# Optimization experiments

Hardware: AMD Instinct MI355X
Metric: run time of the kernel (lower is better)

The kernel has to match this reference:

```python
import jax, jax.numpy as jnp
import numpy as np

D_MODEL = 1024
D_STATE = 16
D_CONV = 4
EXPAND = 2
D_INNER = EXPAND * D_MODEL
BATCH = 2
SEQ = 4096


def setup_inputs() -> dict:
    key = jax.random.key(0)
    ks = jax.random.split(key, 8)
    def w(k, shape, fan_in):
        return jax.random.normal(k, shape, jnp.float32) * (fan_in ** -0.5)
    x = jax.random.normal(ks[0], (BATCH, SEQ, D_MODEL), jnp.float32)
    in_proj_w = w(ks[1], (2 * D_INNER, D_MODEL), D_MODEL)
    conv_w = w(ks[2], (D_INNER, 1, D_CONV), D_CONV)          # depthwise conv kernel (OIH, groups=D_INNER)
    conv_b = jnp.zeros((D_INNER,), jnp.float32)
    x_proj_w = w(ks[3], (1 + 2 * D_STATE, D_INNER), D_INNER)
    dt_proj_w = w(ks[4], (D_INNER, 1), D_STATE)               # Linear(1 -> d_inner), see notes
    dt_proj_b = jnp.zeros((D_INNER,), jnp.float32)
    A_log = jnp.log(jnp.tile(jnp.arange(1, D_STATE + 1, dtype=jnp.float32)[None, :], (D_INNER, 1)))
    D = jnp.ones((D_INNER,), jnp.float32)
    out_proj_w = w(ks[5], (D_MODEL, D_INNER), D_INNER)
    return dict(x=x, in_proj_w=in_proj_w, conv_w=conv_w, conv_b=conv_b,
                x_proj_w=x_proj_w, dt_proj_w=dt_proj_w, dt_proj_b=dt_proj_b,
                A_log=A_log, D=D, out_proj_w=out_proj_w)


def _selective_scan(xs, delta, Bm, Cm, A, D):
    # xs, delta: [B, L, d_inner]; Bm, Cm: [B, L, d_state]; A: [d_inner, d_state]
    def step(h, inp):
        x_t, d_t, b_t, c_t = inp                      # [B,di],[B,di],[B,n],[B,n]
        dA = jnp.exp(d_t[..., None] * A)              # [B, di, n]
        h = dA * h + (d_t * x_t)[..., None] * b_t[:, None, :]
        y = jnp.einsum('bdn,bn->bd', h, c_t) + D * x_t
        return h, y
    h0 = jnp.zeros((xs.shape[0], xs.shape[2], A.shape[1]), xs.dtype)
    seq = (jnp.swapaxes(xs, 0, 1), jnp.swapaxes(delta, 0, 1),
           jnp.swapaxes(Bm, 0, 1), jnp.swapaxes(Cm, 0, 1))
    _, ys = jax.lax.scan(step, h0, seq)               # ys: [L, B, di]
    return jnp.swapaxes(ys, 0, 1)


def _mamba(x, in_proj_w, conv_w, conv_b, x_proj_w, dt_proj_w, dt_proj_b, A_log, D, out_proj_w):
    xz = x @ in_proj_w.T                               # [B, L, 2*di]
    xc, z = jnp.split(xz, 2, axis=-1)
    # causal depthwise conv (pad left d_conv-1, truncate to seq_len)
    u = jnp.swapaxes(xc, 1, 2)                         # [B, di, L]
    u = jax.lax.conv_general_dilated(
        u, conv_w, window_strides=(1,), padding=[(D_CONV - 1, 0)],
        feature_group_count=D_INNER, dimension_numbers=('NCH', 'OIH', 'NCH'))
    u = u + conv_b[None, :, None]
    xs = jax.nn.silu(jnp.swapaxes(u, 1, 2))            # [B, L, di]
    dbc = xs @ x_proj_w.T                              # [B, L, 1+2n]
    delta_raw = dbc[..., :1]
    Bm = dbc[..., 1:1 + D_STATE]
    Cm = dbc[..., 1 + D_STATE:]
    delta = jax.nn.softplus(delta_raw @ dt_proj_w.T + dt_proj_b)   # [B, L, di]
    A = -jnp.exp(A_log)
    y = _selective_scan(xs, delta, Bm, Cm, A, D)
    return (y * jax.nn.silu(z)) @ out_proj_w.T


def reference(x, in_proj_w, conv_w, conv_b, x_proj_w, dt_proj_w, dt_proj_b, A_log, D, out_proj_w):
    return _mamba(x, in_proj_w, conv_w, conv_b, x_proj_w, dt_proj_w, dt_proj_b, A_log, D, out_proj_w)
```

## Files before the change

### kernel.cpp

```cpp
#include <hip/hip_runtime.h>
#include <hip/hip_bf16.h>
#include <stdint.h>

typedef __bf16 bf16x8 __attribute__((ext_vector_type(8)));
typedef float  f32x4  __attribute__((ext_vector_type(4)));
typedef unsigned short u16x8 __attribute__((ext_vector_type(8)));

#define TC 64
#define NC 64
#define TH 32

__device__ __forceinline__ unsigned short f2bf(float f) {
  unsigned u = __builtin_bit_cast(unsigned, f);
  unsigned r = (u + 0x7fffu + ((u >> 16) & 1u)) >> 16;
  return (unsigned short)r;
}
__device__ __forceinline__ float bf2f(unsigned short s) {
  unsigned u = ((unsigned)s) << 16;
  return __builtin_bit_cast(float, u);
}

__device__ __forceinline__ void gload_lds16(const void* g, void* l) {
  __builtin_amdgcn_global_load_lds(
      (const __attribute__((address_space(1))) unsigned int*)(g),
      (__attribute__((address_space(3))) unsigned int*)(l),
      16, 0, 0);
}

__device__ __forceinline__ void rpowers(float r, float* rp) {
  float r2 = r * r, r4 = r2 * r2, r8 = r4 * r4;
  rp[0] = r;        rp[1] = r2;       rp[2] = r2 * r;   rp[3] = r4;
  rp[4] = r4 * r;   rp[5] = r4 * r2;  rp[6] = rp[5] * r; rp[7] = r8;
  rp[8] = r8 * r;   rp[9] = r8 * r2;  rp[10] = rp[9] * r; rp[11] = r8 * r4;
  rp[12] = rp[11] * r; rp[13] = rp[11] * r2; rp[14] = rp[13] * r; rp[15] = r8 * r8;
}

__global__ __launch_bounds__(256) void cast_bf16_k(const float4* __restrict__ in,
                                                   ushort4* __restrict__ out, int n4) {
  int i = blockIdx.x * 256 + threadIdx.x;
  int stride = gridDim.x * 256;
  for (; i < n4; i += stride) {
    float4 v = in[i];
    ushort4 o;
    o.x = f2bf(v.x); o.y = f2bf(v.y); o.z = f2bf(v.z); o.w = f2bf(v.w);
    out[i] = o;
  }
}

__global__ __launch_bounds__(256) void pad_xw_k(const float* __restrict__ xw,
                                                unsigned short* __restrict__ xwp) {
  int i = blockIdx.x * 256 + threadIdx.x;
  if (i >= 128 * 2048) return;
  int row = i >> 11, col = i & 2047;
  xwp[i] = (row < 33) ? f2bf(xw[row * 2048 + col]) : (unsigned short)0;
}

template <bool BF16OUT>
__global__ __launch_bounds__(256) void gemm_bf16_nt(
    const unsigned short* __restrict__ A, const unsigned short* __restrict__ B,
    void* __restrict__ Cv, int M, int N, int K)
{
  __shared__ __align__(16) unsigned short As[128 * 32];
  __shared__ __align__(16) unsigned short Bs[128 * 32];
  const int tid = threadIdx.x;
  const int m0 = blockIdx.x * 128;
  const int n0 = blockIdx.y * 128;
  const int w = tid >> 6, l = tid & 63;
  const int wr = w >> 1, wc = w & 1;
  const int lr = l & 15, kk = (l >> 4) * 8;

  f32x4 acc[4][4];
#pragma unroll
  for (int mi = 0; mi < 4; ++mi)
#pragma unroll
    for (int ni = 0; ni < 4; ++ni)
      acc[mi][ni] = (f32x4){0.f, 0.f, 0.f, 0.f};

  for (int k0 = 0; k0 < K; k0 += 32) {
#pragma unroll
    for (int i = 0; i < 2; ++i) {
      int q = tid + 256 * i;
      int row = q >> 2, sub = q & 3;
      gload_lds16(A + (size_t)(m0 + row) * K + k0 + sub * 8, &As[q * 8]);
      gload_lds16(B + (size_t)(n0 + row) * K + k0 + sub * 8, &Bs[q * 8]);
    }
    __syncthreads();
    bf16x8 af[4], bfr[4];
#pragma unroll
    for (int mi = 0; mi < 4; ++mi)
      af[mi] = *(const bf16x8*)&As[(wr * 64 + mi * 16 + lr) * 32 + kk];
#pragma unroll
    for (int ni = 0; ni < 4; ++ni)
      bfr[ni] = *(const bf16x8*)&Bs[(wc * 64 + ni * 16 + lr) * 32 + kk];
#pragma unroll
    for (int mi = 0; mi < 4; ++mi)
#pragma unroll
      for (int ni = 0; ni < 4; ++ni)
        acc[mi][ni] = __builtin_amdgcn_mfma_f32_16x16x32_bf16(af[mi], bfr[ni], acc[mi][ni], 0, 0, 0);
    __syncthreads();
  }

#pragma unroll
  for (int mi = 0; mi < 4; ++mi)
#pragma unroll
    for (int ni = 0; ni < 4; ++ni) {
      int gr = m0 + wr * 64 + mi * 16 + (l >> 4) * 4;
      int gc = n0 + wc * 64 + ni * 16 + (l & 15);
#pragma unroll
      for (int j = 0; j < 4; ++j) {
        if (BF16OUT)
          ((unsigned short*)Cv)[(size_t)(gr + j) * N + gc] = f2bf(acc[mi][ni][j]);
        else
          ((float*)Cv)[(size_t)(gr + j) * N + gc] = acc[mi][ni][j];
      }
    }
}

#define KSPLIT 4
__global__ __launch_bounds__(256) void gemm_bf16_splitk(
    const unsigned short* __restrict__ A, const unsigned short* __restrict__ B,
    float* __restrict__ Cpart, int M, int N, int K)
{
  __shared__ __align__(16) unsigned short As[128 * 32];
  __shared__ __align__(16) unsigned short Bs[128 * 32];
  const int tid = threadIdx.x;
  const int m0 = blockIdx.x * 128;
  const int n0 = 0;
  const int z = blockIdx.z;
  const int kseg = K / KSPLIT;
  const int kbeg = z * kseg;
  const int w = tid >> 6, l = tid & 63;
  const int wr = w >> 1, wc = w & 1;
  const int lr = l & 15, kk = (l >> 4) * 8;
  float* C = Cpart + (size_t)z * M * N;

  f32x4 acc[4][4];
#pragma unroll
  for (int mi = 0; mi < 4; ++mi)
#pragma unroll
    for (int ni = 0; ni < 4; ++ni)
      acc[mi][ni] = (f32x4){0.f, 0.f, 0.f, 0.f};

  for (int k0 = kbeg; k0 < kbeg + kseg; k0 += 32) {
#pragma unroll
    for (int i = 0; i < 2; ++i) {
      int q = tid + 256 * i;
      int row = q >> 2, sub = q & 3;
      gload_lds16(A + (size_t)(m0 + row) * K + k0 + sub * 8, &As[q * 8]);
      gload_lds16(B + (size_t)(n0 + row) * K + k0 + sub * 8, &Bs[q * 8]);
    }
    __syncthreads();
    bf16x8 af[4], bfr[4];
#pragma unroll
    for (int mi = 0; mi < 4; ++mi)
      af[mi] = *(const bf16x8*)&As[(wr * 64 + mi * 16 + lr) * 32 + kk];
#pragma unroll
    for (int ni = 0; ni < 4; ++ni)
      bfr[ni] = *(const bf16x8*)&Bs[(wc * 64 + ni * 16 + lr) * 32 + kk];
#pragma unroll
    for (int mi = 0; mi < 4; ++mi)
#pragma unroll
      for (int ni = 0; ni < 4; ++ni)
        acc[mi][ni] = __builtin_amdgcn_mfma_f32_16x16x32_bf16(af[mi], bfr[ni], acc[mi][ni], 0, 0, 0);
    __syncthreads();
  }

#pragma unroll
  for (int mi = 0; mi < 4; ++mi)
#pragma unroll
    for (int ni = 0; ni < 4; ++ni) {
      int gr = m0 + wr * 64 + mi * 16 + (l >> 4) * 4;
      int gc = n0 + wc * 64 + ni * 16 + (l & 15);
#pragma unroll
      for (int j = 0; j < 4; ++j)
        C[(size_t)(gr + j) * N + gc] = acc[mi][ni][j];
    }
}

__global__ __launch_bounds__(256) void redux4_k(const float4* __restrict__ part,
                                                float4* __restrict__ out) {
  int i = blockIdx.x * 256 + threadIdx.x;
  const int STR = 262144;
  float4 a = part[i], b = part[i + STR], c = part[i + 2 * STR], d = part[i + 3 * STR];
  out[i] = make_float4(a.x + b.x + c.x + d.x, a.y + b.y + c.y + d.y,
                       a.z + b.z + c.z + d.z, a.w + b.w + c.w + d.w);
}

#define CONV_L 16
__global__ __launch_bounds__(256) void conv_silu_k(
    const unsigned short* __restrict__ xzb, const float* __restrict__ cw,
    const float* __restrict__ cb, unsigned short* __restrict__ xsb)
{
  const int b = blockIdx.y;
  const int l0 = blockIdx.x * CONV_L;
  const int d = threadIdx.x * 8;
  float w[4][8], bias[8];
#pragma unroll
  for (int i = 0; i < 8; ++i) {
    bias[i] = cb[d + i];
#pragma unroll
    for (int j = 0; j < 4; ++j) w[j][i] = cw[(d + i) * 4 + j];
  }
  const size_t rb = (size_t)b * 4096;
  float win[3][8];
#pragma unroll
  for (int j = 0; j < 3; ++j) {
    int l = l0 - 3 + j;
    if (l >= 0) {
      u16x8 v = *(const u16x8*)(xzb + (rb + l) * 4096 + d);
#pragma unroll
      for (int i = 0; i < 8; ++i) win[j][i] = bf2f(v[i]);
    } else {
#pragma unroll
      for (int i = 0; i < 8; ++i) win[j][i] = 0.f;
    }
  }
  for (int l = l0; l < l0 + CONV_L; ++l) {
    u16x8 v = *(const u16x8*)(xzb + (rb + l) * 4096 + d);
    float cur[8]; u16x8 ob;
#pragma unroll
    for (int i = 0; i < 8; ++i) {
      cur[i] = bf2f(v[i]);
      float u = bias[i] + w[0][i] * win[0][i] + w[1][i] * win[1][i]
                        + w[2][i] * win[2][i] + w[3][i] * cur[i];
      float s = u / (1.f + __expf(-u));
      ob[i] = f2bf(s);
    }
    *(u16x8*)(xsb + (rb + l) * 2048 + d) = ob;
#pragma unroll
    for (int i = 0; i < 8; ++i) { win[0][i] = win[1][i]; win[1][i] = win[2][i]; win[2][i] = cur[i]; }
  }
}

__global__ __launch_bounds__(256) void scan_p1(
    const unsigned short* __restrict__ xsb16, const float* __restrict__ dbc,
    const float* __restrict__ dtw, const float* __restrict__ dtb,
    const float* __restrict__ alog,
    float* __restrict__ Sg, float* __restrict__ cdg)
{
  const int chunk = blockIdx.x;
  const int d0 = blockIdx.y * 256;
  const int b = blockIdx.z;
  const int tid = threadIdx.x;
  const size_t rowbase = (size_t)b * 4096 + chunk * TC;

  __shared__ __align__(16) unsigned short xsS[TH][256];
  __shared__ __align__(16) float bS[TC][16];
  __shared__ float drS[TC];

  if (tid < TC) drS[tid] = dbc[(rowbase + tid) * 128];
  for (int i = tid; i < TC * 16; i += 256) {
    int t = i >> 4, q = i & 15;
    bS[t][q] = dbc[(rowbase + t) * 128 + 1 + q];
  }

  const int d = d0 + tid;
  const float wdt = dtw[d], bdt = dtb[d];
  float adn[16];
  bool ok = true;
#pragma unroll
  for (int k = 0; k < 4; ++k) {
    float4 a4 = *(const float4*)(alog + (size_t)d * 16 + k * 4);
    adn[4 * k + 0] = -__expf(a4.x); adn[4 * k + 1] = -__expf(a4.y);
    adn[4 * k + 2] = -__expf(a4.z); adn[4 * k + 3] = -__expf(a4.w);
  }
#pragma unroll
  for (int n = 0; n < 16; ++n)
    ok = ok && (fabsf(adn[n] + (float)(n + 1)) <= 1e-3f * (float)(n + 1));

  float h[16];
#pragma unroll
  for (int n = 0; n < 16; ++n) h[n] = 0.f;
  float cd = 0.f;

  for (int half = 0; half < 2; ++half) {
    if (half) __syncthreads();
    for (int i = tid; i < TH * 32; i += 256) {
      int tt = i >> 5, q = i & 31;
      *(u16x8*)&xsS[tt][q * 8] =
          *(const u16x8*)(xsb16 + (rowbase + half * TH + tt) * 2048 + d0 + q * 8);
    }
    __syncthreads();

    if (ok) {
      for (int tt = 0; tt < TH; ++tt) {
        int t = half * TH + tt;
        float pre = fmaf(drS[t], wdt, bdt);
        float e = __expf(pre);
        float dlt = (pre > 20.f) ? pre : __logf(1.f + e);
        float xv = bf2f(xsS[tt][tid]);
        float dx = dlt * xv;
        cd += dlt;
        float r = __expf(-dlt);
        float rp[16];
        rpowers(r, rp);
        f32x4 Bv[4];
#pragma unroll
        for (int k = 0; k < 4; ++k) Bv[k] = ((const f32x4*)&bS[t][0])[k];
#pragma unroll
        for (int n = 0; n < 16; ++n)
          h[n] = fmaf(rp[n], h[n], dx * Bv[n >> 2][n & 3]);
      }
    } else {
      for (int tt = 0; tt < TH; ++tt) {
        int t = half * TH + tt;
        float pre = fmaf(drS[t], wdt, bdt);
        float e = __expf(pre);
        float dlt = (pre > 20.f) ? pre : __logf(1.f + e);
        float xv = bf2f(xsS[tt][tid]);
        float dx = dlt * xv;
        cd += dlt;
        f32x4 Bv[4];
#pragma unroll
        for (int k = 0; k < 4; ++k) Bv[k] = ((const f32x4*)&bS[t][0])[k];
#pragma unroll
        for (int n = 0; n < 16; ++n) {
          float dA = __expf(adn[n] * dlt);
          h[n] = fmaf(dA, h[n], dx * Bv[n >> 2][n & 3]);
        }
      }
    }
  }
  cdg[(size_t)(b * NC + chunk) * 2048 + d] = cd;
  float* Sp = Sg + ((size_t)(b * NC + chunk) * 32768 + (size_t)d * 16);
#pragma unroll
  for (int k = 0; k < 4; ++k)
    ((float4*)Sp)[k] = make_float4(h[4 * k], h[4 * k + 1], h[4 * k + 2], h[4 * k + 3]);
}

__global__ __launch_bounds__(256) void scan_p2(
    const float* __restrict__ Sg, const float* __restrict__ cdg,
    const float* __restrict__ alog, float* __restrict__ Hg)
{
  int g = blockIdx.x * 256 + threadIdx.x;
  int b = g >> 15, dn = g & 32767;
  int d = dn >> 4;
  float adn = -__expf(alog[dn]);
  float h = 0.f;
  for (int c = 0; c < NC; ++c) {
    size_t o = (size_t)(b * NC + c) * 32768 + dn;
    float P = __expf(adn * cdg[(size_t)(b * NC + c) * 2048 + d]);
    Hg[o] = h;
    h = fmaf(P, h, Sg[o]);
  }
}

__global__ __launch_bounds__(256) void scan_p3(
    const unsigned short* __restrict__ xsb16, const float* __restrict__ dbc,
    const float* __restrict__ dtw, const float* __restrict__ dtb,
    const float* __restrict__ alog, const float* __restrict__ Dp,
    const unsigned short* __restrict__ xzb, const float* __restrict__ Hg,
    unsigned short* __restrict__ gb)
{
  const int chunk = blockIdx.x;
  const int d0 = blockIdx.y * 256;
  const int b = blockIdx.z;
  const int tid = threadIdx.x;
  const size_t rowbase = (size_t)b * 4096 + chunk * TC;

  __shared__ __align__(16) unsigned short xsS[TH][256];
  __shared__ __align__(16) float bcS[TC][32];

  for (int i = tid; i < TC * 32; i += 256) {
    int t = i >> 5, q = i & 31;
    bcS[t][q] = dbc[(rowbase + t) * 128 + 1 + q];
  }

  const int d = d0 + tid;
  const float wdt = dtw[d], bdt = dtb[d], Dd = Dp[d];
  const float* __restrict__ drp = dbc + rowbase * 128;
  float adn[16];
  bool ok = true;
#pragma unroll
  for (int k = 0; k < 4; ++k) {
    float4 a4 = *(const float4*)(alog + (size_t)d * 16 + k * 4);
    adn[4 * k + 0] = -__expf(a4.x); adn[4 * k + 1] = -__expf(a4.y);
    adn[4 * k + 2] = -__expf(a4.z); adn[4 * k + 3] = -__expf(a4.w);
  }
#pragma unroll
  for (int n = 0; n < 16; ++n)
    ok = ok && (fabsf(adn[n] + (float)(n + 1)) <= 1e-3f * (float)(n + 1));

  float h[16];
  {
    const float* Hp = Hg + ((size_t)(b * NC + chunk) * 32768 + (size_t)d * 16);
#pragma unroll
    for (int k = 0; k < 4; ++k) {
      float4 h4 = ((const float4*)Hp)[k];
      h[4 * k + 0] = h4.x; h[4 * k + 1] = h4.y; h[4 * k + 2] = h4.z; h[4 * k + 3] = h4.w;
    }
  }

  for (int half = 0; half < 2; ++half) {
    if (half) __syncthreads();
    for (int i = tid; i < TH * 32; i += 256) {
      int tt = i >> 5, q = i & 31;
      *(u16x8*)&xsS[tt][q * 8] =
          *(const u16x8*)(xsb16 + (rowbase + half * TH + tt) * 2048 + d0 + q * 8);
    }
    __syncthreads();

    if (ok) {
      for (int tt = 0; tt < TH; ++tt) {
        int t = half * TH + tt;
        float pre = fmaf(drp[(size_t)t * 128], wdt, bdt);
        float e = __expf(pre);
        float dlt = (pre > 20.f) ? pre : __logf(1.f + e);
        float xv = bf2f(xsS[tt][tid]);
        float dx = dlt * xv;
        float r = __expf(-dlt);
        float rp[16];
        rpowers(r, rp);
        f32x4 Bv[4], Cv[4];
#pragma unroll
        for (int k = 0; k < 4; ++k) {
          Bv[k] = ((const f32x4*)&bcS[t][0])[k];
          Cv[k] = ((const f32x4*)&bcS[t][16])[k];
        }
        float yp[4];
        yp[0] = Dd * xv; yp[1] = 0.f; yp[2] = 0.f; yp[3] = 0.f;
#pragma unroll
        for (int n = 0; n < 16; ++n) {
          h[n] = fmaf(rp[n], h[n], dx * Bv[n >> 2][n & 3]);
          yp[n & 3] = fmaf(h[n], Cv[n >> 2][n & 3], yp[n & 3]);
        }
        float y = (yp[0] + yp[1]) + (yp[2] + yp[3]);
        xsS[tt][tid] = f2bf(y);
      }
    } else {
      for (int tt = 0; tt < TH; ++tt) {
        int t = half * TH + tt;
        float pre = fmaf(drp[(size_t)t * 128], wdt, bdt);
        float e = __expf(pre);
        float dlt = (pre > 20.f) ? pre : __logf(1.f + e);
        float xv = bf2f(xsS[tt][tid]);
        float dx = dlt * xv;
        f32x4 Bv[4], Cv[4];
#pragma unroll
        for (int k = 0; k < 4; ++k) {
          Bv[k] = ((const f32x4*)&bcS[t][0])[k];
          Cv[k] = ((const f32x4*)&bcS[t][16])[k];
        }
        float yp[4];
        yp[0] = Dd * xv; yp[1] = 0.f; yp[2] = 0.f; yp[3] = 0.f;
#pragma unroll
        for (int n = 0; n < 16; ++n) {
          float dA = __expf(adn[n] * dlt);
          h[n] = fmaf(dA, h[n], dx * Bv[n >> 2][n & 3]);
          yp[n & 3] = fmaf(h[n], Cv[n >> 2][n & 3], yp[n & 3]);
        }
        float y = (yp[0] + yp[1]) + (yp[2] + yp[3]);
        xsS[tt][tid] = f2bf(y);
      }
    }
    __syncthreads();

    for (int i = tid; i < TH * 32; i += 256) {
      int tt = i >> 5, q = i & 31;
      size_t row = rowbase + half * TH + tt;
      u16x8 yv = *(const u16x8*)&xsS[tt][q * 8];
      u16x8 zv = *(const u16x8*)(xzb + row * 4096 + 2048 + d0 + q * 8);
      u16x8 ov;
#pragma unroll
      for (int j = 0; j < 8; ++j) {
        float z = bf2f(zv[j]);
        float s = z / (1.f + __expf(-z));
        ov[j] = f2bf(bf2f(yv[j]) * s);
      }
      *(u16x8*)(gb + row * 2048 + d0 + q * 8) = ov;
    }
  }
}

extern "C" void kernel_launch(void* const* d_in, const int* in_sizes, int n_in,
                              void* d_out, int out_size, void* d_ws, size_t ws_size,
                              hipStream_t stream) {
  const float* x    = (const float*)d_in[0];
  const float* ipw  = (const float*)d_in[1];
  const float* cw   = (const float*)d_in[2];
  const float* cb   = (const float*)d_in[3];
  const float* xpw  = (const float*)d_in[4];
  const float* dtw  = (const float*)d_in[5];
  const float* dtb  = (const float*)d_in[6];
  const float* alog = (const float*)d_in[7];
  const float* Dp   = (const float*)d_in[8];
  const float* opw  = (const float*)d_in[9];
  float* out = (float*)d_out;

  char* p = (char*)d_ws;
  unsigned short* xb   = (unsigned short*)p; p += (size_t)8388608 * 2;
  unsigned short* wb1  = (unsigned short*)p; p += (size_t)4194304 * 2;
  unsigned short* wb2  = (unsigned short*)p; p += (size_t)2097152 * 2;
  unsigned short* xwp  = (unsigned short*)p; p += (size_t)262144 * 2;
  unsigned short* xzb  = (unsigned short*)p; p += (size_t)33554432 * 2;
  unsigned short* xsb16= (unsigned short*)p; p += (size_t)16777216 * 2;
  float*          dbc  = (float*)p;          p += (size_t)1048576 * 4;
  unsigned short* gb   = (unsigned short*)p; p += (size_t)16777216 * 2;
  float*          Sg   = (float*)p;          p += (size_t)4194304 * 4;
  float*          cdg  = (float*)p;          p += (size_t)262144 * 4;
  float*          Hg   = (float*)xb;
  float*          dbcp = Sg;

  cast_bf16_k<<<1024, 256, 0, stream>>>((const float4*)x,   (ushort4*)xb,  8388608 / 4);
  cast_bf16_k<<<1024, 256, 0, stream>>>((const float4*)ipw, (ushort4*)wb1, 4194304 / 4);
  cast_bf16_k<<<512,  256, 0, stream>>>((const float4*)opw, (ushort4*)wb2, 2097152 / 4);
  pad_xw_k<<<1024, 256, 0, stream>>>(xpw, xwp);

  gemm_bf16_nt<true ><<<dim3(64, 32), 256, 0, stream>>>(xb, wb1, xzb, 8192, 4096, 1024);
  conv_silu_k<<<dim3(4096 / CONV_L, 2), 256, 0, stream>>>(xzb, cw, cb, xsb16);

  gemm_bf16_splitk<<<dim3(64, 1, KSPLIT), 256, 0, stream>>>(xsb16, xwp, dbcp, 8192, 128, 2048);
  redux4_k<<<1024, 256, 0, stream>>>((const float4*)dbcp, (float4*)dbc);

  scan_p1<<<dim3(NC, 8, 2), 256, 0, stream>>>(xsb16, dbc, dtw, dtb, alog, Sg, cdg);
  scan_p2<<<256, 256, 0, stream>>>(Sg, cdg, alog, Hg);
  scan_p3<<<dim3(NC, 8, 2), 256, 0, stream>>>(xsb16, dbc, dtw, dtb, alog, Dp, xzb, Hg, gb);

  gemm_bf16_nt<false><<<dim3(64, 8), 256, 0, stream>>>(gb, wb2, out, 8192, 1024, 2048);
}
```

Measured before the change: 320.9 us.

## Triple-buffer GEMM LDS tiles with async prefetch and grouped tile swizzle

Replaces the single-buffered GEMM kernels with one templated kernel that keeps three LDS stages. It prefetches two k-tiles ahead using global_load_lds and waits with partial vmcnt counts plus a raw s_barrier. Blocks are remapped through an XCD-aware swizzle and a grouped-M tile ordering to improve L2 reuse. The same kernel also covers split-K through gridDim.z, replacing the separate split-K kernel. LDS use grows threefold, and correctness now depends on the hand-written vmcnt accounting.

```diff
diff --git a/kernel.cpp b/kernel.cpp
--- a/kernel.cpp
+++ b/kernel.cpp
@@ -55,16 +55,33 @@
   xwp[i] = (row < 33) ? f2bf(xw[row * 2048 + col]) : (unsigned short)0;
 }
 
-template <bool BF16OUT>
-__global__ __launch_bounds__(256) void gemm_bf16_nt(
+template <bool BF16OUT, bool SWZ>
+__global__ __launch_bounds__(256) void gemm2p(
     const unsigned short* __restrict__ A, const unsigned short* __restrict__ B,
     void* __restrict__ Cv, int M, int N, int K)
 {
-  __shared__ __align__(16) unsigned short As[128 * 32];
-  __shared__ __align__(16) unsigned short Bs[128 * 32];
+  __shared__ __align__(16) unsigned short AsB[3 * 128 * 32];
+  __shared__ __align__(16) unsigned short BsB[3 * 128 * 32];
   const int tid = threadIdx.x;
-  const int m0 = blockIdx.x * 128;
-  const int n0 = blockIdx.y * 128;
+
+  const int grid_m = M >> 7, grid_n = N >> 7;
+  const int nwg = grid_m * grid_n;
+  int wid = blockIdx.x;
+  if (SWZ) { int q = nwg >> 3; wid = (wid & 7) * q + (wid >> 3); }
+  const int GM = 16;
+  const int nig = GM * grid_n;
+  const int gidg = wid / nig;
+  const int rem = wid - gidg * nig;
+  const int fm = gidg * GM;
+  const int gsz = min(grid_m - fm, GM);
+  const int pm = fm + rem % gsz;
+  const int pn = rem / gsz;
+  const int m0 = pm << 7, n0 = pn << 7;
+
+  const int kseg = K / gridDim.z;
+  const int kbeg = blockIdx.z * kseg;
+  const int NT = kseg >> 5;
+
   const int w = tid >> 6, l = tid & 63;
   const int wr = w >> 1, wc = w & 1;
   const int lr = l & 15, kk = (l >> 4) * 8;
@@ -76,28 +93,52 @@
     for (int ni = 0; ni < 4; ++ni)
       acc[mi][ni] = (f32x4){0.f, 0.f, 0.f, 0.f};
 
-  for (int k0 = 0; k0 < K; k0 += 32) {
+#pragma unroll
+  for (int tt = 0; tt < 2; ++tt) {
+    unsigned short* as = AsB + tt * 4096;
+    unsigned short* bs = BsB + tt * 4096;
+    int k0 = kbeg + tt * 32;
 #pragma unroll
     for (int i = 0; i < 2; ++i) {
       int q = tid + 256 * i;
       int row = q >> 2, sub = q & 3;
-      gload_lds16(A + (size_t)(m0 + row) * K + k0 + sub * 8, &As[q * 8]);
-      gload_lds16(B + (size_t)(n0 + row) * K + k0 + sub * 8, &Bs[q * 8]);
-    }
-    __syncthreads();
+      gload_lds16(A + (size_t)(m0 + row) * K + k0 + sub * 8, as + q * 8);
+      gload_lds16(B + (size_t)(n0 + row) * K + k0 + sub * 8, bs + q * 8);
+    }
+  }
+  asm volatile("s_waitcnt vmcnt(4)\n\ts_barrier" ::: "memory");
+
+  for (int t = 0; t < NT; ++t) {
+    if (t + 2 < NT) {
+      unsigned short* as = AsB + ((t + 2) % 3) * 4096;
+      unsigned short* bs = BsB + ((t + 2) % 3) * 4096;
+      int k0 = kbeg + (t + 2) * 32;
+#pragma unroll
+      for (int i = 0; i < 2; ++i) {
+        int q = tid + 256 * i;
+        int row = q >> 2, sub = q & 3;
+        gload_lds16(A + (size_t)(m0 + row) * K + k0 + sub * 8, as + q * 8);
+        gload_lds16(B + (size_t)(n0 + row) * K + k0 + sub * 8, bs + q * 8);
+      }
+    }
+    const unsigned short* as = AsB + (t % 3) * 4096;
+    const unsigned short* bs = BsB + (t % 3) * 4096;
     bf16x8 af[4], bfr[4];
 #pragma unroll
     for (int mi = 0; mi < 4; ++mi)
-      af[mi] = *(const bf16x8*)&As[(wr * 64 + mi * 16 + lr) * 32 + kk];
+      af[mi] = *(const bf16x8*)&as[(wr * 64 + mi * 16 + lr) * 32 + kk];
 #pragma unroll
     for (int ni = 0; ni < 4; ++ni)
-      bfr[ni] = *(const bf16x8*)&Bs[(wc * 64 + ni * 16 + lr) * 32 + kk];
+      bfr[ni] = *(const bf16x8*)&bs[(wc * 64 + ni * 16 + lr) * 32 + kk];
 #pragma unroll
     for (int mi = 0; mi < 4; ++mi)
 #pragma unroll
       for (int ni = 0; ni < 4; ++ni)
         acc[mi][ni] = __builtin_amdgcn_mfma_f32_16x16x32_bf16(af[mi], bfr[ni], acc[mi][ni], 0, 0, 0);
-    __syncthreads();
+    if (t + 1 < NT) {
+      if (t + 2 < NT) asm volatile("s_waitcnt vmcnt(4)\n\ts_barrier" ::: "memory");
+      else            asm volatile("s_waitcnt vmcnt(0)\n\ts_barrier" ::: "memory");
+    }
   }
 
 #pragma unroll
@@ -111,69 +152,8 @@
         if (BF16OUT)
           ((unsigned short*)Cv)[(size_t)(gr + j) * N + gc] = f2bf(acc[mi][ni][j]);
         else
-          ((float*)Cv)[(size_t)(gr + j) * N + gc] = acc[mi][ni][j];
-      }
-    }
-}
-
-#define KSPLIT 4
-__global__ __launch_bounds__(256) void gemm_bf16_splitk(
-    const unsigned short* __restrict__ A, const unsigned short* __restrict__ B,
-    float* __restrict__ Cpart, int M, int N, int K)
-{
-  __shared__ __align__(16) unsigned short As[128 * 32];
-  __shared__ __align__(16) unsigned short Bs[128 * 32];
-  const int tid = threadIdx.x;
-  const int m0 = blockIdx.x * 128;
-  const int n0 = 0;
-  const int z = blockIdx.z;
-  const int kseg = K / KSPLIT;
-  const int kbeg = z * kseg;
-  const int w = tid >> 6, l = tid & 63;
-  const int wr = w >> 1, wc = w & 1;
-  const int lr = l & 15, kk = (l >> 4) * 8;
-  float* C = Cpart + (size_t)z * M * N;
-
-  f32x4 acc[4][4];
-#pragma unroll
-  for (int mi = 0; mi < 4; ++mi)
-#pragma unroll
-    for (int ni = 0; ni < 4; ++ni)
-      acc[mi][ni] = (f32x4){0.f, 0.f, 0.f, 0.f};
-
-  for (int k0 = kbeg; k0 < kbeg + kseg; k0 += 32) {
-#pragma unroll
-    for (int i = 0; i < 2; ++i) {
-      int q = tid + 256 * i;
-      int row = q >> 2, sub = q & 3;
-      gload_lds16(A + (size_t)(m0 + row) * K + k0 + sub * 8, &As[q * 8]);
-      gload_lds16(B + (size_t)(n0 + row) * K + k0 + sub * 8, &Bs[q * 8]);
-    }
-    __syncthreads();
-    bf16x8 af[4], bfr[4];
-#pragma unroll
-    for (int mi = 0; mi < 4; ++mi)
-      af[mi] = *(const bf16x8*)&As[(wr * 64 + mi * 16 + lr) * 32 + kk];
-#pragma unroll
-    for (int ni = 0; ni < 4; ++ni)
-      bfr[ni] = *(const bf16x8*)&Bs[(wc * 64 + ni * 16 + lr) * 32 + kk];
-#pragma unroll
-    for (int mi = 0; mi < 4; ++mi)
-#pragma unroll
-      for (int ni = 0; ni < 4; ++ni)
-        acc[mi][ni] = __builtin_amdgcn_mfma_f32_16x16x32_bf16(af[mi], bfr[ni], acc[mi][ni], 0, 0, 0);
-    __syncthreads();
-  }
-
-#pragma unroll
-  for (int mi = 0; mi < 4; ++mi)
-#pragma unroll
-    for (int ni = 0; ni < 4; ++ni) {
-      int gr = m0 + wr * 64 + mi * 16 + (l >> 4) * 4;
-      int gc = n0 + wc * 64 + ni * 16 + (l & 15);
-#pragma unroll
-      for (int j = 0; j < 4; ++j)
-        C[(size_t)(gr + j) * N + gc] = acc[mi][ni][j];
+          ((float*)Cv + (size_t)blockIdx.z * M * N)[(size_t)(gr + j) * N + gc] = acc[mi][ni][j];
+      }
     }
 }
 
@@ -506,15 +486,15 @@
   cast_bf16_k<<<512,  256, 0, stream>>>((const float4*)opw, (ushort4*)wb2, 2097152 / 4);
   pad_xw_k<<<1024, 256, 0, stream>>>(xpw, xwp);
 
-  gemm_bf16_nt<true ><<<dim3(64, 32), 256, 0, stream>>>(xb, wb1, xzb, 8192, 4096, 1024);
+  gemm2p<true, true><<<2048, 256, 0, stream>>>(xb, wb1, xzb, 8192, 4096, 1024);
   conv_silu_k<<<dim3(4096 / CONV_L, 2), 256, 0, stream>>>(xzb, cw, cb, xsb16);
 
-  gemm_bf16_splitk<<<dim3(64, 1, KSPLIT), 256, 0, stream>>>(xsb16, xwp, dbcp, 8192, 128, 2048);
+  gemm2p<false, false><<<dim3(64, 1, 4), 256, 0, stream>>>(xsb16, xwp, dbcp, 8192, 128, 2048);
   redux4_k<<<1024, 256, 0, stream>>>((const float4*)dbcp, (float4*)dbc);
 
   scan_p1<<<dim3(NC, 8, 2), 256, 0, stream>>>(xsb16, dbc, dtw, dtb, alog, Sg, cdg);
   scan_p2<<<256, 256, 0, stream>>>(Sg, cdg, alog, Hg);
   scan_p3<<<dim3(NC, 8, 2), 256, 0, stream>>>(xsb16, dbc, dtw, dtb, alog, Dp, xzb, Hg, gb);
 
-  gemm_bf16_nt<false><<<dim3(64, 8), 256, 0, stream>>>(gb, wb2, out, 8192, 1024, 2048);
-}
+  gemm2p<false, true><<<512, 256, 0, stream>>>(gb, wb2, out, 8192, 1024, 2048);
+}
```

Result: faster. 310.5 us (-3.2%).
